# Kernel tuning notes

Hardware: AMD Instinct MI355X
Metric: run time of the kernel (lower is better)

## Reference

```python
import jax, jax.numpy as jnp
import numpy as np

P, H_OUT, D, NX = 32, 1, 256, 16
S_A = -0.1

def layernorm(x, g, b, eps=1e-5):
    mu = jnp.mean(x, axis=-1, keepdims=True)
    var = jnp.var(x, axis=-1, keepdims=True)
    return (x - mu) * jax.lax.rsqrt(var + eps) * g + b

def setup_inputs() -> dict:
    key = jax.random.key(0)
    ks = jax.random.split(key, 16)
    B, L = 8, 2048
    y = jax.random.normal(ks[0], (B, L, P), jnp.float32)
    Win = jax.random.normal(ks[1], (P, D), jnp.float32) / np.sqrt(P)
    bin_ = jnp.zeros((D,), jnp.float32)
    ng = jnp.ones((D,), jnp.float32); nb = jnp.zeros((D,), jnp.float32)
    # A = -10*rand + s_A, with A[:,0] = s_A (fix first state of each channel)
    A = -10.0 * jax.random.uniform(ks[2], (D, NX), jnp.float32) + S_A
    A = A.at[:, 0].set(S_A)
    W_B = jax.random.normal(ks[3], (NX, D), jnp.float32)
    W_C = jax.random.normal(ks[4], (NX, D), jnp.float32)
    q_delta = jax.random.normal(ks[5], (D,), jnp.float32)
    p_delta = jax.random.normal(ks[6], (1,), jnp.float32)
    nfg = jnp.ones((D,), jnp.float32); nfb = jnp.zeros((D,), jnp.float32)
    W1 = jax.random.normal(ks[7], (D, D), jnp.float32) / np.sqrt(D)
    b1 = jnp.zeros((D,), jnp.float32)
    W2 = jax.random.normal(ks[8], (D, H_OUT * P), jnp.float32) / np.sqrt(D)
    b2 = jnp.zeros((H_OUT * P,), jnp.float32)
    return {"y": y, "Win": Win, "bin_": bin_, "ng": ng, "nb": nb, "A": A,
            "W_B": W_B, "W_C": W_C, "q_delta": q_delta, "p_delta": p_delta,
            "nfg": nfg, "nfb": nfb, "W1": W1, "b1": b1, "W2": W2, "b2": b2}

def selective_scan(u, delta, A, Bm, Cm):
    # u: (B,L,D), delta: (B,L), A: (D,NX), Bm/Cm: (B,L,NX)
    dA = jnp.exp(delta[..., None, None] * A)                      # (B,L,D,NX)
    dBu = delta[..., None, None] * Bm[:, :, None, :] * u[..., None]  # (B,L,D,NX)
    x0 = jnp.zeros((u.shape[0], u.shape[2], A.shape[1]), u.dtype)
    def step(x, inp):
        dA_t, dBu_t, C_t = inp
        x = dA_t * x + dBu_t                                      # (B,D,NX)
        y_t = jnp.einsum('bdn,bn->bd', x, C_t)
        return x, y_t
    _, ys = jax.lax.scan(step, x0, (dA.transpose(1, 0, 2, 3),
                                    dBu.transpose(1, 0, 2, 3),
                                    Cm.transpose(1, 0, 2)))
    return ys.transpose(1, 0, 2)                                  # (B,L,D)

def reference(y, Win, bin_, ng, nb, A, W_B, W_C, q_delta, p_delta,
              nfg, nfb, W1, b1, W2, b2):
    B, L, _ = y.shape
    h = y @ Win + bin_                                            # (B,L,D)
    hn = layernorm(h, ng, nb)
    delta = jax.nn.softplus(p_delta[0] + jnp.einsum('bld,d->bl', hn, q_delta))
    Bm = jnp.einsum('nd,bld->bln', W_B, hn)
    Cm = jnp.einsum('nd,bld->bln', W_C, hn)
    upd = selective_scan(hn, delta, A, Bm, Cm)
    h = h + upd
    h = layernorm(h, nfg, nfb)
    out = jax.nn.gelu(h @ W1 + b1, approximate=False) @ W2 + b2
    return out.reshape(B, L, H_OUT, P)
```

## Files before the change

kernel.cpp:

```cpp
#include <hip/hip_runtime.h>
#include <math.h>

#define D 256
#define NX 16
#define L 2048
#define NBATCH 8
#define NTOK (NBATCH * L)
#define CL 32
#define NCH (L / CL)
#define LOG2E 1.44269504088896340736f

typedef float f32x4 __attribute__((ext_vector_type(4)));
typedef short bf16x8 __attribute__((ext_vector_type(8)));

__device__ __forceinline__ unsigned short f2bf(float x) {
  unsigned u = __float_as_uint(x);
  u = u + 0x7fffu + ((u >> 16) & 1u);
  return (unsigned short)(u >> 16);
}
__device__ __forceinline__ float bf2f(unsigned short h) {
  return __uint_as_float(((unsigned)h) << 16);
}

__global__ __launch_bounds__(256) void k0_prep(const float* __restrict__ A,
                                               const float* __restrict__ WB,
                                               const float* __restrict__ WC,
                                               const float* __restrict__ Win,
                                               const float* __restrict__ W1,
                                               const float* __restrict__ W2,
                                               const float* __restrict__ nfg,
                                               const float* __restrict__ nfb,
                                               float* __restrict__ At,
                                               unsigned short* __restrict__ W1fh,
                                               unsigned short* __restrict__ W1fl,
                                               unsigned short* __restrict__ W2fh,
                                               unsigned short* __restrict__ W2fl,
                                               unsigned short* __restrict__ Winfh,
                                               unsigned short* __restrict__ Winfl,
                                               unsigned short* __restrict__ Wbcfh,
                                               unsigned short* __restrict__ Wbcfl,
                                               float* __restrict__ u1,
                                               float* __restrict__ v1) {
  int i = blockIdx.x * 256 + threadIdx.x;
  if (i < 4096) {
    int d = i >> 4, n = i & 15;
    At[n * D + d] = A[i] * LOG2E;
  } else if (i < 12288) {
    int e = i - 4096;
    int j = e & 7, l = (e >> 3) & 63, tt = e >> 9;
    int k = ((l >> 4) << 3) + j;
    int n = tt * 16 + (l & 15);
    float x = Win[k * 256 + n];
    unsigned short h = f2bf(x);
    Winfh[e] = h;
    Winfl[e] = f2bf(x - bf2f(h));
  } else if (i < 20480) {
    int e = i - 12288;
    int j = e & 7, l = (e >> 3) & 63, q = e >> 9;
    int s = q >> 1, tt = q & 1;
    int k = s * 32 + ((l >> 4) << 3) + j;
    int n = tt * 16 + (l & 15);
    float x = (n < 16) ? WB[n * 256 + k] : WC[(n - 16) * 256 + k];
    unsigned short h = f2bf(x);
    Wbcfh[e] = h;
    Wbcfl[e] = f2bf(x - bf2f(h));
  } else if (i < 86016) {
    int e = i - 20480;
    int j = e & 7, l = (e >> 3) & 63, tt = (e >> 9) & 15, s = e >> 13;
    int k = s * 32 + ((l >> 4) << 3) + j;
    int n = tt * 16 + (l & 15);
    float x = W1[k * 256 + n] * nfg[k];
    unsigned short h = f2bf(x);
    W1fh[e] = h;
    W1fl[e] = f2bf(x - bf2f(h));
  } else if (i < 94208) {
    int e = i - 86016;
    int j = e & 7, l = (e >> 3) & 63, tt = (e >> 9) & 1, s = e >> 10;
    int k = s * 32 + ((l >> 4) << 3) + j;
    int n = tt * 16 + (l & 15);
    float x = W2[k * 32 + n];
    unsigned short h = f2bf(x);
    W2fh[e] = h;
    W2fl[e] = f2bf(x - bf2f(h));
  } else if (i < 94464) {
    int c = i - 94208;
    float s = 0.f;
    for (int d = 0; d < 256; ++d) s += nfg[d] * W1[d * 256 + c];
    u1[c] = s;
  } else if (i < 94720) {
    int c = i - 94464;
    float s = 0.f;
    for (int d = 0; d < 256; ++d) s += nfb[d] * W1[d * 256 + c];
    v1[c] = s;
  }
}

__global__ __launch_bounds__(512, 4) void k1a_front_scan(
    const float* __restrict__ y, const float* __restrict__ bin_,
    const float* __restrict__ ng, const float* __restrict__ nb,
    const float* __restrict__ qd, const float* __restrict__ pd,
    const float* __restrict__ At,
    const unsigned short* __restrict__ Winfh,
    const unsigned short* __restrict__ Winfl,
    const unsigned short* __restrict__ Wbcfh,
    const unsigned short* __restrict__ Wbcfl,
    float* __restrict__ vpart, float* __restrict__ cdsg,
    float* __restrict__ Cm,
    float* __restrict__ EX, float* __restrict__ T) {
  __shared__ float sy[32][36];
  __shared__ float sh[32][260];
  __shared__ float sB[32][NX];
  __shared__ float sC[32][NX];
  __shared__ float sred[32][16];
  __shared__ float sdelta[32];
  __shared__ float smu[32];
  __shared__ float srstd[32];
  __shared__ float ssig[32];
  __shared__ __align__(16) unsigned short sChA_h[32 * 256];
  __shared__ __align__(16) unsigned short sChA_l[32 * 256];
  int t = threadIdx.x;
  int l = t & 63;
  int w = t >> 6;
  int tok0 = blockIdx.x * 32;
  if (t < 256) {
    *(float4*)&sy[t >> 3][(t & 7) * 4] =
        ((const float4*)(y + (size_t)tok0 * 32))[t];
  }
  __syncthreads();
  f32x4 acc[2][2];
  {
    bf16x8 yah[2], yal[2];
    int k0 = (l >> 4) << 3;
    #pragma unroll
    for (int m = 0; m < 2; ++m) {
      int row = m * 16 + (l & 15);
      float4 f0 = *(float4*)&sy[row][k0];
      float4 f1 = *(float4*)&sy[row][k0 + 4];
      float v0 = f0.x, v1_ = f0.y, v2 = f0.z, v3 = f0.w;
      float v4 = f1.x, v5 = f1.y, v6 = f1.z, v7 = f1.w;
      unsigned short h0 = f2bf(v0), h1 = f2bf(v1_), h2 = f2bf(v2), h3 = f2bf(v3);
      unsigned short h4 = f2bf(v4), h5 = f2bf(v5), h6 = f2bf(v6), h7 = f2bf(v7);
      yah[m][0] = (short)h0; yah[m][1] = (short)h1; yah[m][2] = (short)h2; yah[m][3] = (short)h3;
      yah[m][4] = (short)h4; yah[m][5] = (short)h5; yah[m][6] = (short)h6; yah[m][7] = (short)h7;
      yal[m][0] = (short)f2bf(v0 - bf2f(h0)); yal[m][1] = (short)f2bf(v1_ - bf2f(h1));
      yal[m][2] = (short)f2bf(v2 - bf2f(h2)); yal[m][3] = (short)f2bf(v3 - bf2f(h3));
      yal[m][4] = (short)f2bf(v4 - bf2f(h4)); yal[m][5] = (short)f2bf(v5 - bf2f(h5));
      yal[m][6] = (short)f2bf(v6 - bf2f(h6)); yal[m][7] = (short)f2bf(v7 - bf2f(h7));
    }
    const bf16x8* Bh = (const bf16x8*)Winfh;
    const bf16x8* Bl = (const bf16x8*)Winfl;
    #pragma unroll
    for (int n = 0; n < 2; ++n) {
      int tt = w * 2 + n;
      bf16x8 bh = Bh[tt * 64 + l];
      bf16x8 bl = Bl[tt * 64 + l];
      #pragma unroll
      for (int m = 0; m < 2; ++m) {
        f32x4 a = {0.f, 0.f, 0.f, 0.f};
        a = __builtin_amdgcn_mfma_f32_16x16x32_bf16(yah[m], bh, a, 0, 0, 0);
        a = __builtin_amdgcn_mfma_f32_16x16x32_bf16(yal[m], bh, a, 0, 0, 0);
        a = __builtin_amdgcn_mfma_f32_16x16x32_bf16(yah[m], bl, a, 0, 0, 0);
        a = __builtin_amdgcn_mfma_f32_16x16x32_bf16(yal[m], bl, a, 0, 0, 0);
        acc[m][n] = a;
      }
    }
  }
  int c0 = w * 32 + (l & 15), c1 = c0 + 16;
  {
    float b0 = bin_[c0], b1v = bin_[c1];
    #pragma unroll
    for (int m = 0; m < 2; ++m)
      #pragma unroll
      for (int r = 0; r < 4; ++r) { acc[m][0][r] += b0; acc[m][1][r] += b1v; }
  }
  {
    #pragma unroll
    for (int m = 0; m < 2; ++m)
      #pragma unroll
      for (int r = 0; r < 4; ++r) {
        float a0 = acc[m][0][r], a1 = acc[m][1][r];
        float s1 = a0 + a1;
        float s2 = a0 * a0 + a1 * a1;
        #pragma unroll
        for (int off = 1; off < 16; off <<= 1) {
          s1 += __shfl_xor(s1, off);
          s2 += __shfl_xor(s2, off);
        }
        if ((l & 15) == 0) {
          int tok = m * 16 + ((l >> 4) << 2) + r;
          sred[tok][w * 2] = s1;
          sred[tok][w * 2 + 1] = s2;
        }
      }
  }
  __syncthreads();
  if (t < 32) {
    float s1 = 0.f, s2 = 0.f;
    #pragma unroll
    for (int q = 0; q < 8; ++q) { s1 += sred[t][q * 2]; s2 += sred[t][q * 2 + 1]; }
    float mu = s1 * (1.f / D);
    float var = s2 * (1.f / D) - mu * mu;
    float rstd = rsqrtf(var + 1e-5f);
    smu[t] = mu;
    srstd[t] = rstd;
    ssig[t] = sqrtf(var + 1e-5f);
  }
  __syncthreads();
  {
    float g0 = ng[c0], g1 = ng[c1];
    float nb0 = nb[c0], nb1 = nb[c1];
    float q0 = qd[c0], q1 = qd[c1];
    float ddv[2][4];
    #pragma unroll
    for (int m = 0; m < 2; ++m)
      #pragma unroll
      for (int r = 0; r < 4; ++r) {
        int tok = m * 16 + ((l >> 4) << 2) + r;
        float mu = smu[tok], rstd = srstd[tok];
        float h0 = (acc[m][0][r] - mu) * rstd * g0 + nb0;
        float h1 = (acc[m][1][r] - mu) * rstd * g1 + nb1;
        sh[tok][c0] = h0;
        sh[tok][c1] = h1;
        float dx = h0 * q0 + h1 * q1;
        #pragma unroll
        for (int off = 1; off < 16; off <<= 1) dx += __shfl_xor(dx, off);
        ddv[m][r] = dx;
      }
    if ((l & 15) == 0) {
      #pragma unroll
      for (int m = 0; m < 2; ++m)
        #pragma unroll
        for (int r = 0; r < 4; ++r)
          sred[m * 16 + ((l >> 4) << 2) + r][w] = ddv[m][r];
    }
  }
  __syncthreads();
  if (t < 32) {
    float dsum = 0.f;
    #pragma unroll
    for (int q = 0; q < 8; ++q) dsum += sred[t][q];
    float xx = pd[0] + dsum;
    float dv = (xx > 20.f) ? xx : log1pf(expf(xx));
    sdelta[t] = dv;
    float c = dv;
    #pragma unroll
    for (int off = 1; off < 32; off <<= 1) {
      float o = __shfl_up(c, off);
      if (t >= off) c += o;
    }
    cdsg[tok0 + t] = c;
    if (t == 31) T[blockIdx.x] = c;
  }
  {
    int row = t & 31;
    int cq = (t >> 5) * 16;
    float4 f0 = *(float4*)&sh[row][cq];
    float4 f1 = *(float4*)&sh[row][cq + 4];
    float4 f2 = *(float4*)&sh[row][cq + 8];
    float4 f3 = *(float4*)&sh[row][cq + 12];
    float vv[16] = {f0.x, f0.y, f0.z, f0.w, f1.x, f1.y, f1.z, f1.w,
                    f2.x, f2.y, f2.z, f2.w, f3.x, f3.y, f3.z, f3.w};
    unsigned hw[8], lw[8];
    #pragma unroll
    for (int p = 0; p < 8; ++p) {
      unsigned short ha = f2bf(vv[2 * p]), hb = f2bf(vv[2 * p + 1]);
      unsigned short la = f2bf(vv[2 * p] - bf2f(ha));
      unsigned short lb = f2bf(vv[2 * p + 1] - bf2f(hb));
      hw[p] = (unsigned)ha | ((unsigned)hb << 16);
      lw[p] = (unsigned)la | ((unsigned)lb << 16);
    }
    unsigned base = (unsigned)row * 512;
    #pragma unroll
    for (int g = 0; g < 2; ++g) {
      unsigned off = ((unsigned)(cq * 2 + g * 16)) ^ ((unsigned)(row & 7) << 4);
      uint4 hv4 = {hw[g * 4], hw[g * 4 + 1], hw[g * 4 + 2], hw[g * 4 + 3]};
      uint4 lv4 = {lw[g * 4], lw[g * 4 + 1], lw[g * 4 + 2], lw[g * 4 + 3]};
      *(uint4*)((char*)sChA_h + base + off) = hv4;
      *(uint4*)((char*)sChA_l + base + off) = lv4;
    }
  }
  __syncthreads();
  if (w < 4) {
    int mw = w & 1, nw = w >> 1;
    int row = mw * 16 + (l & 15);
    unsigned abase = (unsigned)row * 512;
    const bf16x8* B2h = (const bf16x8*)Wbcfh;
    const bf16x8* B2l = (const bf16x8*)Wbcfl;
    f32x4 acc2 = {0.f, 0.f, 0.f, 0.f};
    #pragma unroll
    for (int s = 0; s < 8; ++s) {
      unsigned off = ((unsigned)(s * 64 + ((l >> 4) << 4))) ^ ((unsigned)(row & 7) << 4);
      bf16x8 ah = *(const bf16x8*)((const char*)sChA_h + abase + off);
      bf16x8 al = *(const bf16x8*)((const char*)sChA_l + abase + off);
      int bi = (s * 2 + nw) * 64 + l;
      bf16x8 bh = B2h[bi];
      bf16x8 bl = B2l[bi];
      acc2 = __builtin_amdgcn_mfma_f32_16x16x32_bf16(ah, bh, acc2, 0, 0, 0);
      acc2 = __builtin_amdgcn_mfma_f32_16x16x32_bf16(al, bh, acc2, 0, 0, 0);
      acc2 = __builtin_amdgcn_mfma_f32_16x16x32_bf16(ah, bl, acc2, 0, 0, 0);
      acc2 = __builtin_amdgcn_mfma_f32_16x16x32_bf16(al, bl, acc2, 0, 0, 0);
    }
    int tokr = mw * 16 + ((l >> 4) << 2);
    int colc = l & 15;
    if (nw == 0) {
      #pragma unroll
      for (int r = 0; r < 4; ++r) sB[tokr + r][colc] = acc2[r];
    } else {
      #pragma unroll
      for (int r = 0; r < 4; ++r) {
        Cm[(size_t)(tok0 + tokr + r) * NX + colc] = acc2[r];
        sC[tokr + r][colc] = acc2[r];
      }
    }
  }
  __syncthreads();
  if (t < 256) {
    int d = t;
    float a16v[16], x16v[16];
    size_t exbase = (size_t)blockIdx.x * (NX * D) + d;
    #pragma unroll
    for (int n = 0; n < 16; ++n) {
      a16v[n] = At[n * D + d];
      x16v[n] = 0.f;
    }
    float nb_d = nb[d];
    float invg = 1.0f / ng[d];
    float* vout = vpart + (size_t)tok0 * D + d;
    for (int lo = 0; lo < CL; ++lo) {
      float hnv = sh[lo][d];
      float dlt = sdelta[lo];
      float du = dlt * hnv;
      float Bv[16], Cvv[16];
      *(float4*)&Bv[0]  = *(float4*)&sB[lo][0];
      *(float4*)&Bv[4]  = *(float4*)&sB[lo][4];
      *(float4*)&Bv[8]  = *(float4*)&sB[lo][8];
      *(float4*)&Bv[12] = *(float4*)&sB[lo][12];
      *(float4*)&Cvv[0]  = *(float4*)&sC[lo][0];
      *(float4*)&Cvv[4]  = *(float4*)&sC[lo][4];
      *(float4*)&Cvv[8]  = *(float4*)&sC[lo][8];
      *(float4*)&Cvv[12] = *(float4*)&sC[lo][12];
      float p = 0.f;
      #pragma unroll
      for (int n = 0; n < 16; ++n) {
        x16v[n] = fmaf(exp2f(dlt * a16v[n]), x16v[n], du * Bv[n]);
        p = fmaf(x16v[n], Cvv[n], p);
      }
      float h = fmaf((hnv - nb_d) * invg, ssig[lo], smu[lo]);
      vout[(size_t)lo * D] = h + p;
    }
    #pragma unroll
    for (int n = 0; n < 16; ++n) EX[exbase + n * D] = x16v[n];
  }
}

__global__ __launch_bounds__(64) void k2b_chunkscan(
    const float* __restrict__ At, const float* __restrict__ T,
    float* __restrict__ EX) {
  __shared__ float sT[NCH];
  int b = blockIdx.x >> 6;
  int rem = ((blockIdx.x & 63) << 6) | threadIdx.x;
  sT[threadIdx.x] = T[b * NCH + threadIdx.x];
  __syncthreads();
  float A2 = At[rem];
  size_t base = ((size_t)b << 18) + rem;
  float eq[8];
  #pragma unroll
  for (int j = 0; j < 8; ++j) eq[j] = EX[base + ((size_t)j << 12)];
  float x = 0.f;
  #pragma unroll 8
  for (int c = 0; c < NCH; ++c) {
    float e = eq[c & 7];
    if (c + 8 < NCH) eq[c & 7] = EX[base + ((size_t)(c + 8) << 12)];
    EX[base + ((size_t)c << 12)] = x;
    x = fmaf(exp2f(sT[c] * A2), x, e);
  }
}

__device__ __forceinline__ float gelu_exact(float x) {
  return 0.5f * x * (1.f + erff(x * 0.70710678118654752440f));
}

__global__ __launch_bounds__(512, 4) void k2cd_scan_mlp(
    const float* __restrict__ vpart, const float* __restrict__ cdsg,
    const float* __restrict__ Cm,
    const float* __restrict__ At, const float* __restrict__ EX,
    const unsigned short* __restrict__ W1fh, const unsigned short* __restrict__ W1fl,
    const unsigned short* __restrict__ W2fh, const unsigned short* __restrict__ W2fl,
    const float* __restrict__ u1, const float* __restrict__ v1,
    const float* __restrict__ b1, const float* __restrict__ b2,
    float* __restrict__ out) {
  __shared__ __align__(16) unsigned short sAh[32 * 256];
  __shared__ __align__(16) unsigned short sAl[32 * 256];
  __shared__ float srstd2[32];
  __shared__ float smur2[32];
  int t = threadIdx.x;
  int l = t & 63, w = t >> 6;
  int tok0 = blockIdx.x * 32;
  size_t tokbase = (size_t)tok0;
  {
    int g = t >> 8, d = t & 255;
    float a16v[16], xe[16];
    size_t exbase = (size_t)blockIdx.x * (NX * D) + d;
    #pragma unroll
    for (int n = 0; n < 16; ++n) {
      a16v[n] = At[n * D + d];
      xe[n] = EX[exbase + n * D];
    }
    const float* vp_base = vpart + (tokbase + g * 16) * D + d;
    #pragma unroll 4
    for (int q = 0; q < 16; ++q) {
      int tok = g * 16 + q;
      float vp = vp_base[(size_t)q * D];
      float ct = cdsg[tokbase + tok];
      float pf = 0.f;
      #pragma unroll
      for (int n = 0; n < 16; ++n) {
        float cv = Cm[(tokbase + tok) * NX + n];
        pf = fmaf(cv * exp2f(ct * a16v[n]), xe[n], pf);
      }
      float v = vp + pf;
      unsigned short vh = f2bf(v);
      unsigned short vl = f2bf(v - bf2f(vh));
      unsigned off16 = ((unsigned)(d * 2)) ^ ((unsigned)((tok & 7) << 4));
      *(unsigned short*)((char*)sAh + tok * 512 + off16) = vh;
      *(unsigned short*)((char*)sAl + tok * 512 + off16) = vl;
    }
  }
  __syncthreads();
  {
    #pragma unroll
    for (int p = 0; p < 4; ++p) {
      int tok = w * 4 + p;
      unsigned off = ((unsigned)(l * 8)) ^ ((unsigned)((tok & 7) << 4));
      uint2 hv2 = *(uint2*)((char*)sAh + tok * 512 + off);
      uint2 lv2 = *(uint2*)((char*)sAl + tok * 512 + off);
      float v0 = bf2f((unsigned short)(hv2.x & 0xffff)) + bf2f((unsigned short)(lv2.x & 0xffff));
      float v1_ = bf2f((unsigned short)(hv2.x >> 16)) + bf2f((unsigned short)(lv2.x >> 16));
      float v2 = bf2f((unsigned short)(hv2.y & 0xffff)) + bf2f((unsigned short)(lv2.y & 0xffff));
      float v3 = bf2f((unsigned short)(hv2.y >> 16)) + bf2f((unsigned short)(lv2.y >> 16));
      float s1 = v0 + v1_ + v2 + v3;
      float s2 = v0 * v0 + v1_ * v1_ + v2 * v2 + v3 * v3;
      #pragma unroll
      for (int off2 = 1; off2 < 64; off2 <<= 1) {
        s1 += __shfl_xor(s1, off2);
        s2 += __shfl_xor(s2, off2);
      }
      if (l == 0) {
        float mu = s1 * (1.f / D);
        float var = s2 * (1.f / D) - mu * mu;
        float rstd = rsqrtf(var + 1e-5f);
        srstd2[tok] = rstd;
        smur2[tok] = mu * rstd;
      }
    }
  }
  __syncthreads();
  const bf16x8* B1h = (const bf16x8*)W1fh;
  const bf16x8* B1l = (const bf16x8*)W1fl;
  f32x4 acc[2][2];
  #pragma unroll
  for (int m = 0; m < 2; ++m)
    #pragma unroll
    for (int n = 0; n < 2; ++n) {
      f32x4 z4 = {0.f, 0.f, 0.f, 0.f};
      acc[m][n] = z4;
    }
  #pragma unroll 2
  for (int s = 0; s < 8; ++s) {
    bf16x8 ah[2], al[2];
    #pragma unroll
    for (int m = 0; m < 2; ++m) {
      int row = m * 16 + (l & 15);
      unsigned off16 = ((unsigned)(s * 64 + ((l >> 4) << 4))) ^ ((unsigned)(row & 7) << 4);
      ah[m] = *(const bf16x8*)((const char*)sAh + row * 512 + off16);
      al[m] = *(const bf16x8*)((const char*)sAl + row * 512 + off16);
    }
    #pragma unroll
    for (int n = 0; n < 2; ++n) {
      int bi = (s * 16 + w * 2 + n) * 64 + l;
      bf16x8 bh = B1h[bi];
      bf16x8 bl = B1l[bi];
      #pragma unroll
      for (int m = 0; m < 2; ++m) {
        acc[m][n] = __builtin_amdgcn_mfma_f32_16x16x32_bf16(ah[m], bh, acc[m][n], 0, 0, 0);
        acc[m][n] = __builtin_amdgcn_mfma_f32_16x16x32_bf16(al[m], bh, acc[m][n], 0, 0, 0);
        acc[m][n] = __builtin_amdgcn_mfma_f32_16x16x32_bf16(ah[m], bl, acc[m][n], 0, 0, 0);
        acc[m][n] = __builtin_amdgcn_mfma_f32_16x16x32_bf16(al[m], bl, acc[m][n], 0, 0, 0);
      }
    }
  }
  __syncthreads();
  #pragma unroll
  for (int n = 0; n < 2; ++n) {
    int colz = w * 32 + n * 16 + (l & 15);
    float u1c = u1[colz];
    float v1c = v1[colz] + b1[colz];
    #pragma unroll
    for (int m = 0; m < 2; ++m) {
      #pragma unroll
      for (int r = 0; r < 4; ++r) {
        int row = m * 16 + ((l >> 4) << 2) + r;
        float zpre = acc[m][n][r] * srstd2[row] - smur2[row] * u1c + v1c;
        float zv = gelu_exact(zpre);
        unsigned short zh = f2bf(zv);
        unsigned short zl = f2bf(zv - bf2f(zh));
        unsigned off16 = ((unsigned)(colz * 2)) ^ ((unsigned)(row & 7) << 4);
        *(unsigned short*)((char*)sAh + row * 512 + off16) = zh;
        *(unsigned short*)((char*)sAl + row * 512 + off16) = zl;
      }
    }
  }
  __syncthreads();
  if (w < 4) {
    int mw = w >> 1, nw = w & 1;
    const bf16x8* B2h = (const bf16x8*)W2fh;
    const bf16x8* B2l = (const bf16x8*)W2fl;
    f32x4 acc2 = {0.f, 0.f, 0.f, 0.f};
    #pragma unroll 2
    for (int s = 0; s < 8; ++s) {
      int row = mw * 16 + (l & 15);
      unsigned off16 = ((unsigned)(s * 64 + ((l >> 4) << 4))) ^ ((unsigned)(row & 7) << 4);
      bf16x8 zh8 = *(const bf16x8*)((const char*)sAh + row * 512 + off16);
      bf16x8 zl8 = *(const bf16x8*)((const char*)sAl + row * 512 + off16);
      int bi = (s * 2 + nw) * 64 + l;
      bf16x8 bh = B2h[bi];
      bf16x8 bl = B2l[bi];
      acc2 = __builtin_amdgcn_mfma_f32_16x16x32_bf16(zh8, bh, acc2, 0, 0, 0);
      acc2 = __builtin_amdgcn_mfma_f32_16x16x32_bf16(zl8, bh, acc2, 0, 0, 0);
      acc2 = __builtin_amdgcn_mfma_f32_16x16x32_bf16(zh8, bl, acc2, 0, 0, 0);
      acc2 = __builtin_amdgcn_mfma_f32_16x16x32_bf16(zl8, bl, acc2, 0, 0, 0);
    }
    int colo = nw * 16 + (l & 15);
    float b2v = b2[colo];
    #pragma unroll
    for (int r = 0; r < 4; ++r) {
      int row = mw * 16 + ((l >> 4) << 2) + r;
      out[(size_t)(tok0 + row) * 32 + colo] = acc2[r] + b2v;
    }
  }
}

extern "C" void kernel_launch(void* const* d_in, const int* in_sizes, int n_in,
                              void* d_out, int out_size, void* d_ws, size_t ws_size,
                              hipStream_t stream) {
  const float* y    = (const float*)d_in[0];
  const float* Win  = (const float*)d_in[1];
  const float* bin_ = (const float*)d_in[2];
  const float* ng   = (const float*)d_in[3];
  const float* nb   = (const float*)d_in[4];
  const float* A    = (const float*)d_in[5];
  const float* WB   = (const float*)d_in[6];
  const float* WC   = (const float*)d_in[7];
  const float* qd   = (const float*)d_in[8];
  const float* pd   = (const float*)d_in[9];
  const float* nfg  = (const float*)d_in[10];
  const float* nfb  = (const float*)d_in[11];
  const float* W1   = (const float*)d_in[12];
  const float* b1   = (const float*)d_in[13];
  const float* W2   = (const float*)d_in[14];
  const float* b2   = (const float*)d_in[15];

  float* ws = (float*)d_ws;
  float* vpart = ws;
  float* cdsg  = ws + 4194304;
  float* Bm    = cdsg + NTOK;
  float* Cm    = Bm + NTOK * NX;
  float* muv   = Cm + NTOK * NX;
  float* irsv  = muv + NTOK;
  float* Tbuf  = irsv + NTOK;
  float* At    = Tbuf + NBATCH * NCH;
  float* EX    = At + D * NX;
  unsigned short* W1fh  = (unsigned short*)(EX + 2097152);
  unsigned short* W1fl  = W1fh + 65536;
  unsigned short* W2fh  = W1fl + 65536;
  unsigned short* W2fl  = W2fh + 8192;
  unsigned short* Winfh = W2fl + 8192;
  unsigned short* Winfl = Winfh + 8192;
  unsigned short* Wbcfh = Winfl + 8192;
  unsigned short* Wbcfl = Wbcfh + 8192;
  float* u1 = (float*)(Wbcfl + 8192);
  float* v1 = u1 + 256;

  k0_prep<<<370, 256, 0, stream>>>(A, WB, WC, Win, W1, W2, nfg, nfb, At,
                                   W1fh, W1fl, W2fh, W2fl,
                                   Winfh, Winfl, Wbcfh, Wbcfl, u1, v1);
  k1a_front_scan<<<NTOK / 32, 512, 0, stream>>>(y, bin_, ng, nb, qd, pd, At,
                                                Winfh, Winfl, Wbcfh, Wbcfl,
                                                vpart, cdsg, Cm, EX, Tbuf);
  k2b_chunkscan<<<NBATCH * 64, 64, 0, stream>>>(At, Tbuf, EX);
  k2cd_scan_mlp<<<NTOK / 32, 512, 0, stream>>>(vpart, cdsg, Cm, At, EX,
                                               W1fh, W1fl, W2fh, W2fl,
                                               u1, v1, b1, b2, (float*)d_out);
}
```

Measured before the change: 194.5 us.

## Split intra-chunk scan states across both half-blocks and drop fp32 LDS staging

```diff
diff --git a/kernel.cpp b/kernel.cpp
--- a/kernel.cpp
+++ b/kernel.cpp
@@ -95,7 +95,7 @@
   }
 }
 
-__global__ __launch_bounds__(512, 4) void k1a_front_scan(
+__global__ __launch_bounds__(512, 6) void k1a_front_scan(
     const float* __restrict__ y, const float* __restrict__ bin_,
     const float* __restrict__ ng, const float* __restrict__ nb,
     const float* __restrict__ qd, const float* __restrict__ pd,
@@ -104,11 +104,10 @@
     const unsigned short* __restrict__ Winfl,
     const unsigned short* __restrict__ Wbcfh,
     const unsigned short* __restrict__ Wbcfl,
-    float* __restrict__ vpart, float* __restrict__ cdsg,
-    float* __restrict__ Cm,
+    float* __restrict__ vpart0, float* __restrict__ vpart1,
+    float* __restrict__ cdsg, float* __restrict__ Cm,
     float* __restrict__ EX, float* __restrict__ T) {
   __shared__ float sy[32][36];
-  __shared__ float sh[32][260];
   __shared__ float sB[32][NX];
   __shared__ float sC[32][NX];
   __shared__ float sred[32][16];
@@ -219,8 +218,16 @@
         float mu = smu[tok], rstd = srstd[tok];
         float h0 = (acc[m][0][r] - mu) * rstd * g0 + nb0;
         float h1 = (acc[m][1][r] - mu) * rstd * g1 + nb1;
-        sh[tok][c0] = h0;
-        sh[tok][c1] = h1;
+        unsigned swz = (unsigned)((tok & 7) << 4);
+        unsigned base = (unsigned)tok * 512;
+        unsigned short h0h = f2bf(h0);
+        unsigned short h0l = f2bf(h0 - bf2f(h0h));
+        unsigned short h1h = f2bf(h1);
+        unsigned short h1l = f2bf(h1 - bf2f(h1h));
+        *(unsigned short*)((char*)sChA_h + base + (((unsigned)(2 * c0)) ^ swz)) = h0h;
+        *(unsigned short*)((char*)sChA_l + base + (((unsigned)(2 * c0)) ^ swz)) = h0l;
+        *(unsigned short*)((char*)sChA_h + base + (((unsigned)(2 * c1)) ^ swz)) = h1h;
+        *(unsigned short*)((char*)sChA_l + base + (((unsigned)(2 * c1)) ^ swz)) = h1l;
         float dx = h0 * q0 + h1 * q1;
         #pragma unroll
         for (int off = 1; off < 16; off <<= 1) dx += __shfl_xor(dx, off);
@@ -250,34 +257,6 @@
     }
     cdsg[tok0 + t] = c;
     if (t == 31) T[blockIdx.x] = c;
-  }
-  {
-    int row = t & 31;
-    int cq = (t >> 5) * 16;
-    float4 f0 = *(float4*)&sh[row][cq];
-    float4 f1 = *(float4*)&sh[row][cq + 4];
-    float4 f2 = *(float4*)&sh[row][cq + 8];
-    float4 f3 = *(float4*)&sh[row][cq + 12];
-    float vv[16] = {f0.x, f0.y, f0.z, f0.w, f1.x, f1.y, f1.z, f1.w,
-                    f2.x, f2.y, f2.z, f2.w, f3.x, f3.y, f3.z, f3.w};
-    unsigned hw[8], lw[8];
-    #pragma unroll
-    for (int p = 0; p < 8; ++p) {
-      unsigned short ha = f2bf(vv[2 * p]), hb = f2bf(vv[2 * p + 1]);
-      unsigned short la = f2bf(vv[2 * p] - bf2f(ha));
-      unsigned short lb = f2bf(vv[2 * p + 1] - bf2f(hb));
-      hw[p] = (unsigned)ha | ((unsigned)hb << 16);
-      lw[p] = (unsigned)la | ((unsigned)lb << 16);
-    }
-    unsigned base = (unsigned)row * 512;
-    #pragma unroll
-    for (int g = 0; g < 2; ++g) {
-      unsigned off = ((unsigned)(cq * 2 + g * 16)) ^ ((unsigned)(row & 7) << 4);
-      uint4 hv4 = {hw[g * 4], hw[g * 4 + 1], hw[g * 4 + 2], hw[g * 4 + 3]};
-      uint4 lv4 = {lw[g * 4], lw[g * 4 + 1], lw[g * 4 + 2], lw[g * 4 + 3]};
-      *(uint4*)((char*)sChA_h + base + off) = hv4;
-      *(uint4*)((char*)sChA_l + base + off) = lv4;
-    }
   }
   __syncthreads();
   if (w < 4) {
@@ -314,42 +293,47 @@
     }
   }
   __syncthreads();
-  if (t < 256) {
-    int d = t;
-    float a16v[16], x16v[16];
-    size_t exbase = (size_t)blockIdx.x * (NX * D) + d;
-    #pragma unroll
-    for (int n = 0; n < 16; ++n) {
-      a16v[n] = At[n * D + d];
-      x16v[n] = 0.f;
+  {
+    int half = t >> 8;
+    int d = t & 255;
+    float a8[8], x8[8];
+    #pragma unroll
+    for (int n = 0; n < 8; ++n) {
+      a8[n] = At[(half * 8 + n) * D + d];
+      x8[n] = 0.f;
     }
     float nb_d = nb[d];
     float invg = 1.0f / ng[d];
-    float* vout = vpart + (size_t)tok0 * D + d;
+    float* vout = (half ? vpart1 : vpart0) + (size_t)tok0 * D + d;
     for (int lo = 0; lo < CL; ++lo) {
-      float hnv = sh[lo][d];
+      unsigned hoff = ((unsigned)(2 * d)) ^ ((unsigned)((lo & 7) << 4));
+      float hn_v = bf2f(*(unsigned short*)((char*)sChA_h + lo * 512 + hoff)) +
+                   bf2f(*(unsigned short*)((char*)sChA_l + lo * 512 + hoff));
       float dlt = sdelta[lo];
-      float du = dlt * hnv;
-      float Bv[16], Cvv[16];
-      *(float4*)&Bv[0]  = *(float4*)&sB[lo][0];
-      *(float4*)&Bv[4]  = *(float4*)&sB[lo][4];
-      *(float4*)&Bv[8]  = *(float4*)&sB[lo][8];
-      *(float4*)&Bv[12] = *(float4*)&sB[lo][12];
-      *(float4*)&Cvv[0]  = *(float4*)&sC[lo][0];
-      *(float4*)&Cvv[4]  = *(float4*)&sC[lo][4];
-      *(float4*)&Cvv[8]  = *(float4*)&sC[lo][8];
-      *(float4*)&Cvv[12] = *(float4*)&sC[lo][12];
+      float du = dlt * hn_v;
+      float Bv[8], Cvv[8];
+      *(float4*)&Bv[0] = *(float4*)&sB[lo][half * 8];
+      *(float4*)&Bv[4] = *(float4*)&sB[lo][half * 8 + 4];
+      *(float4*)&Cvv[0] = *(float4*)&sC[lo][half * 8];
+      *(float4*)&Cvv[4] = *(float4*)&sC[lo][half * 8 + 4];
       float p = 0.f;
       #pragma unroll
-      for (int n = 0; n < 16; ++n) {
-        x16v[n] = fmaf(exp2f(dlt * a16v[n]), x16v[n], du * Bv[n]);
-        p = fmaf(x16v[n], Cvv[n], p);
-      }
-      float h = fmaf((hnv - nb_d) * invg, ssig[lo], smu[lo]);
-      vout[(size_t)lo * D] = h + p;
-    }
-    #pragma unroll
-    for (int n = 0; n < 16; ++n) EX[exbase + n * D] = x16v[n];
+      for (int n = 0; n < 8; ++n) {
+        x8[n] = fmaf(exp2f(dlt * a8[n]), x8[n], du * Bv[n]);
+        p = fmaf(x8[n], Cvv[n], p);
+      }
+      float v;
+      if (half == 0) {
+        float h = fmaf((hn_v - nb_d) * invg, ssig[lo], smu[lo]);
+        v = h + p;
+      } else {
+        v = p;
+      }
+      vout[(size_t)lo * D] = v;
+    }
+    size_t exbase = (size_t)blockIdx.x * (NX * D) + d;
+    #pragma unroll
+    for (int n = 0; n < 8; ++n) EX[exbase + (half * 8 + n) * D] = x8[n];
   }
 }
 
@@ -381,8 +365,8 @@
 }
 
 __global__ __launch_bounds__(512, 4) void k2cd_scan_mlp(
-    const float* __restrict__ vpart, const float* __restrict__ cdsg,
-    const float* __restrict__ Cm,
+    const float* __restrict__ vpart0, const float* __restrict__ vpart1,
+    const float* __restrict__ cdsg, const float* __restrict__ Cm,
     const float* __restrict__ At, const float* __restrict__ EX,
     const unsigned short* __restrict__ W1fh, const unsigned short* __restrict__ W1fl,
     const unsigned short* __restrict__ W2fh, const unsigned short* __restrict__ W2fl,
@@ -406,11 +390,12 @@
       a16v[n] = At[n * D + d];
       xe[n] = EX[exbase + n * D];
     }
-    const float* vp_base = vpart + (tokbase + g * 16) * D + d;
+    const float* vp0_base = vpart0 + (tokbase + g * 16) * D + d;
+    const float* vp1_base = vpart1 + (tokbase + g * 16) * D + d;
     #pragma unroll 4
     for (int q = 0; q < 16; ++q) {
       int tok = g * 16 + q;
-      float vp = vp_base[(size_t)q * D];
+      float vp = vp0_base[(size_t)q * D] + vp1_base[(size_t)q * D];
       float ct = cdsg[tokbase + tok];
       float pf = 0.f;
       #pragma unroll
@@ -561,13 +546,11 @@
   const float* b2   = (const float*)d_in[15];
 
   float* ws = (float*)d_ws;
-  float* vpart = ws;
-  float* cdsg  = ws + 4194304;
-  float* Bm    = cdsg + NTOK;
-  float* Cm    = Bm + NTOK * NX;
-  float* muv   = Cm + NTOK * NX;
-  float* irsv  = muv + NTOK;
-  float* Tbuf  = irsv + NTOK;
+  float* vpart0 = ws;
+  float* vpart1 = ws + 4194304;
+  float* cdsg  = vpart1 + 4194304;
+  float* Cm    = cdsg + NTOK;
+  float* Tbuf  = Cm + NTOK * NX;
   float* At    = Tbuf + NBATCH * NCH;
   float* EX    = At + D * NX;
   unsigned short* W1fh  = (unsigned short*)(EX + 2097152);
@@ -586,9 +569,11 @@
                                    Winfh, Winfl, Wbcfh, Wbcfl, u1, v1);
   k1a_front_scan<<<NTOK / 32, 512, 0, stream>>>(y, bin_, ng, nb, qd, pd, At,
                                                 Winfh, Winfl, Wbcfh, Wbcfl,
-                                                vpart, cdsg, Cm, EX, Tbuf);
+                                                vpart0, vpart1, cdsg, Cm,
+                                                EX, Tbuf);
   k2b_chunkscan<<<NBATCH * 64, 64, 0, stream>>>(At, Tbuf, EX);
-  k2cd_scan_mlp<<<NTOK / 32, 512, 0, stream>>>(vpart, cdsg, Cm, At, EX,
+  k2cd_scan_mlp<<<NTOK / 32, 512, 0, stream>>>(vpart0, vpart1, cdsg, Cm,
+                                               At, EX,
                                                W1fh, W1fl, W2fh, W2fl,
                                                u1, v1, b1, b2, (float*)d_out);
 }
```

After: 192.0 us. About the same (-1.3%).
